# Kernel tuning notes

Measured on AMD Instinct MI355X. Metric: run time of the kernel, lower is better.

The kernel has to match this reference:

```python
import jax, jax.numpy as jnp
import numpy as np
from jax.scipy.special import ndtr

EPS1 = 1e-6
WEIGHT_DECAY = 1e-5  # FLAGS.weight_decay


def setup_inputs() -> dict:
    key = jax.random.key(0)
    ks = jax.random.split(key, 12)
    B, F, C, Z, S = 512, 512, 500, 64, 100  # batch, features, classes (r_dim), z_dim, n_sample
    lim = np.sqrt(6.0 / (C + Z))
    def glorot(k, shape):
        fan_in, fan_out = shape
        s = np.sqrt(2.0 / (fan_in + fan_out))
        return jax.random.normal(k, shape, jnp.float32) * s
    return {
        "input_X": jax.random.normal(ks[0], (B, F), jnp.float32),
        "input_Y": (jax.random.uniform(ks[1], (B, C)) < 0.1).astype(jnp.float32),  # multi-label targets
        "noise": jax.random.normal(ks[2], (S, B, Z), jnp.float32),
        "W1": glorot(ks[3], (F, 128)), "b1": jnp.zeros((128,), jnp.float32),
        "W2": glorot(ks[4], (128, 256)), "b2": jnp.zeros((256,), jnp.float32),
        "W3": glorot(ks[5], (256, 256)), "b3": jnp.zeros((256,), jnp.float32),
        "Wmu": glorot(ks[6], (256, C)), "bmu": jnp.zeros((C,), jnp.float32),
        "r_sqrt_sigma": jax.random.uniform(ks[7], (C, Z), jnp.float32, -lim, lim),
    }


def reference(input_X, input_Y, noise, W1, b1, W2, b2, W3, b3, Wmu, bmu, r_sqrt_sigma):
    # MLP trunk
    h = jax.nn.relu(input_X @ W1 + b1)
    h = jax.nn.relu(h @ W2 + b2)
    feature = jax.nn.relu(h @ W3 + b3)

    # low-rank covariance: sigma = R R^T, covariance = sigma + I
    cov_diag = jnp.sum(r_sqrt_sigma * r_sqrt_sigma, axis=1) + 1.0  # [C]

    normalized_mu = feature @ Wmu + bmu            # [B, C]
    r_mu = normalized_mu * jnp.sqrt(cov_diag)      # [B, C]

    # MC samples of latent r: [S, B, C]
    sample_r = jnp.einsum('sbz,cz->sbc', noise, r_sqrt_sigma) + r_mu

    E = ndtr(sample_r) * (1.0 - EPS1) + EPS1 * 0.5  # probit CDF, clamped
    # logprob = sum_c [ Y*log(E) + (1-Y)*log(1-E) ]  (== -sum sample_nll)
    logprob = jnp.sum(jnp.log(E) * input_Y + jnp.log1p(-E) * (1.0 - input_Y), axis=2)  # [S, B]
    maxlogprob = jnp.max(logprob, axis=0)                       # [B]
    Eprob = jnp.mean(jnp.exp(logprob - maxlogprob), axis=0)     # [B]
    nll_loss = jnp.mean(-jnp.log(Eprob) - maxlogprob)

    # marginal (independent) probit approximated by scaled sigmoid
    indiv_prob = jax.nn.sigmoid(normalized_mu * 1.70169) * (1.0 - EPS1) + 0.5 * EPS1
    cross_entropy = jnp.log(indiv_prob) * input_Y + jnp.log1p(-indiv_prob) * (1.0 - input_Y)
    marginal_loss = -jnp.mean(jnp.sum(cross_entropy, axis=1))

    l2_loss = WEIGHT_DECAY * (jnp.sum(W1 * W1) + jnp.sum(W2 * W2)
                              + jnp.sum(W3 * W3) + jnp.sum(Wmu * Wmu))
    total_loss = l2_loss + nll_loss
    return indiv_prob, nll_loss, marginal_loss, l2_loss, total_loss
```

## Files before the change

### kernel.cpp

```cpp
#include <hip/hip_runtime.h>
#include <cstddef>

#define EPS1f 1e-6f
#define WDf   1e-5f

constexpr int Bsz = 512, Csz = 500, Zsz = 64, Ssz = 100;

typedef short bf16x8 __attribute__((ext_vector_type(8)));
typedef float f32x4 __attribute__((ext_vector_type(4)));

__device__ inline short f2bf(float f) {
  union { float f; unsigned u; } v; v.f = f;
  unsigned r = (v.u + 0x7fffu + ((v.u >> 16) & 1u)) >> 16;
  return (short)r;
}

__device__ inline float log_probit(float t) {
  const float u = t * -0.70710678118654752f;
  const float au = fabsf(u);
  const float s = __builtin_amdgcn_rcpf(fmaf(0.3275911f, au, 1.f));
  float p = fmaf(1.061405429f, s, -1.453152027f);
  p = fmaf(p, s, 1.421413741f);
  p = fmaf(p, s, -0.284496736f);
  p = fmaf(p, s, 0.254829592f);
  p = p * s;
  const float e = __expf(-au * au);
  const float f = p * e;
  const float erfc_u = (u < 0.f) ? (2.f - f) : f;
  const float E = fmaf(0.5f * erfc_u, 1.f - EPS1f, 0.5f * EPS1f);
  return __logf(E);
}

__device__ inline float block_reduce_sum(float v, float* red) {
  #pragma unroll
  for (int off = 32; off > 0; off >>= 1) v += __shfl_down(v, off, 64);
  const int lane = threadIdx.x & 63, wid = threadIdx.x >> 6;
  if (lane == 0) red[wid] = v;
  __syncthreads();
  float r = 0.f;
  if (threadIdx.x == 0) {
    const int nw = blockDim.x >> 6;
    for (int i = 0; i < nw; ++i) r += red[i];
  }
  __syncthreads();
  return r;
}

__device__ __forceinline__ void gemm32_body(
    const float* __restrict__ A, const float* __restrict__ W,
    const float* __restrict__ bias, float* __restrict__ out,
    int M, int N, int K, int bn0, int bm0, float* As_, float* Ws_, bool relu) {
  const int tid = threadIdx.x;
  const int bn = bn0 * 32, bm = bm0 * 32;
  const int sm = tid >> 3, sk4 = (tid & 7) * 4;
  const int sk = tid >> 3, sn4 = (tid & 7) * 4;
  const int tn = tid & 15, tm = tid >> 4;
  #define AS_(b, k, m) As_[(b) * 1152 + (k) * 36 + (m)]
  #define WS_(b, k, n) Ws_[(b) * 1152 + (k) * 36 + (n)]
  auto loadW = [&](int kt, float4& wv) {
    const float* wrow = W + (size_t)(kt + sk) * N;
    const int nn = bn + sn4;
    if (nn + 3 < N) wv = *reinterpret_cast<const float4*>(wrow + nn);
    else {
      wv.x = (nn + 0 < N) ? wrow[nn + 0] : 0.f;
      wv.y = (nn + 1 < N) ? wrow[nn + 1] : 0.f;
      wv.z = (nn + 2 < N) ? wrow[nn + 2] : 0.f;
      wv.w = (nn + 3 < N) ? wrow[nn + 3] : 0.f;
    }
  };
  {
    float4 av = *reinterpret_cast<const float4*>(A + (size_t)(bm + sm) * K + sk4);
    float4 wv; loadW(0, wv);
    AS_(0, sk4 + 0, sm) = av.x; AS_(0, sk4 + 1, sm) = av.y;
    AS_(0, sk4 + 2, sm) = av.z; AS_(0, sk4 + 3, sm) = av.w;
    *reinterpret_cast<float4*>(&WS_(0, sk, sn4)) = wv;
  }
  __syncthreads();
  float acc[2][2] = {};
  int pb = 0;
  for (int kt = 0; kt < K; kt += 32) {
    const bool more = (kt + 32) < K;
    float4 av2, wv2;
    if (more) {
      av2 = *reinterpret_cast<const float4*>(A + (size_t)(bm + sm) * K + kt + 32 + sk4);
      loadW(kt + 32, wv2);
    }
    #pragma unroll
    for (int k = 0; k < 32; ++k) {
      const float2 a = *reinterpret_cast<const float2*>(&AS_(pb, k, tm * 2));
      const float2 w = *reinterpret_cast<const float2*>(&WS_(pb, k, tn * 2));
      acc[0][0] = fmaf(a.x, w.x, acc[0][0]);
      acc[0][1] = fmaf(a.x, w.y, acc[0][1]);
      acc[1][0] = fmaf(a.y, w.x, acc[1][0]);
      acc[1][1] = fmaf(a.y, w.y, acc[1][1]);
    }
    if (more) {
      const int nb = pb ^ 1;
      AS_(nb, sk4 + 0, sm) = av2.x; AS_(nb, sk4 + 1, sm) = av2.y;
      AS_(nb, sk4 + 2, sm) = av2.z; AS_(nb, sk4 + 3, sm) = av2.w;
      *reinterpret_cast<float4*>(&WS_(nb, sk, sn4)) = wv2;
      __syncthreads();
      pb = nb;
    }
  }
  #pragma unroll
  for (int j = 0; j < 2; ++j) {
    const int n = bn + tn * 2 + j;
    if (n >= N) continue;
    const float bv = bias[n];
    #pragma unroll
    for (int i = 0; i < 2; ++i) {
      const int m = bm + tm * 2 + i;
      float v = acc[i][j] + bv;
      if (relu) v = fmaxf(v, 0.f);
      out[(size_t)m * N + n] = v;
    }
  }
  #undef AS_
  #undef WS_
}

__global__ __launch_bounds__(256) void prep_kernel(
    const float* __restrict__ noise, short* __restrict__ nfB,
    const float* __restrict__ R, short* __restrict__ RbF, float* __restrict__ sqrtcov,
    const float* __restrict__ X, const float* __restrict__ W1,
    const float* __restrict__ b1, float* __restrict__ h1,
    const float* __restrict__ W2, const float* __restrict__ W3,
    const float* __restrict__ Wmu, float* __restrict__ l2_part,
    float* __restrict__ rmuP, float* __restrict__ snP) {
  __shared__ float smem[2304 * 2];
  const int blk = blockIdx.x;
  const int tid = threadIdx.x;
  if (blk < 800) {
    const int g = blk * 256 + tid;
    const int s = g >> 11;
    const int r = g & 2047;
    const int bt = r >> 6;
    const int ln = r & 63;
    const int cl = ln & 15, grp = ln >> 4;
    const float* src = noise + ((size_t)(s * 512 + bt * 16 + cl) * 64 + grp * 8);
    const float4 a = *reinterpret_cast<const float4*>(src);
    const float4 b = *reinterpret_cast<const float4*>(src + 4);
    const float4 c = *reinterpret_cast<const float4*>(src + 32);
    const float4 d = *reinterpret_cast<const float4*>(src + 36);
    bf16x8* dst = reinterpret_cast<bf16x8*>(nfB);
    const int u = (s * 32 + bt) * 128 + ln;
    dst[u]      = bf16x8{ f2bf(a.x), f2bf(a.y), f2bf(a.z), f2bf(a.w),
                          f2bf(b.x), f2bf(b.y), f2bf(b.z), f2bf(b.w) };
    dst[u + 64] = bf16x8{ f2bf(c.x), f2bf(c.y), f2bf(c.z), f2bf(c.w),
                          f2bf(d.x), f2bf(d.y), f2bf(d.z), f2bf(d.w) };
  } else if (blk < 808) {
    const int idx = (blk - 800) * 256 + tid;
    const int c = idx >> 2;
    const int zq = (idx & 3) * 16;
    const bool cv = c < Csz;
    const float* src = R + (size_t)c * Zsz + zq;
    float ss = 0.f;
    if (cv) {
      #pragma unroll
      for (int q = 0; q < 4; ++q) {
        const float4 r4 = *reinterpret_cast<const float4*>(src + q * 4);
        ss = fmaf(r4.x, r4.x, ss); ss = fmaf(r4.y, r4.y, ss);
        ss = fmaf(r4.z, r4.z, ss); ss = fmaf(r4.w, r4.w, ss);
      }
    }
    ss += __shfl_xor(ss, 1, 64);
    ss += __shfl_xor(ss, 2, 64);
    if ((idx & 3) == 0 && cv) sqrtcov[c] = sqrtf(1.f + ss);
  } else if (blk < 824) {
    const int e = (blk - 808) * 256 + tid;
    const int ct = e >> 7;
    const int f = (e >> 6) & 1;
    const int lane = e & 63;
    const int cl = lane & 15, grp = lane >> 4;
    const int c = ct * 16 + cl;
    bf16x8 out = {0, 0, 0, 0, 0, 0, 0, 0};
    if (c < Csz) {
      const float* src = R + (size_t)c * Zsz + f * 32 + grp * 8;
      const float4 a = *reinterpret_cast<const float4*>(src);
      const float4 b = *reinterpret_cast<const float4*>(src + 4);
      out = bf16x8{ f2bf(a.x), f2bf(a.y), f2bf(a.z), f2bf(a.w),
                    f2bf(b.x), f2bf(b.y), f2bf(b.z), f2bf(b.w) };
    }
    reinterpret_cast<bf16x8*>(RbF)[e] = out;
  } else if (blk < 888) {
    const int bid = blk - 824;
    const int gid = bid * 256 + tid;
    const int stride = 64 * 256;
    float s = 0.f;
    for (int i = gid; i < 65536; i += stride) { float v = W1[i]; s = fmaf(v, v, s); }
    for (int i = gid; i < 32768; i += stride) { float v = W2[i]; s = fmaf(v, v, s); }
    for (int i = gid; i < 65536; i += stride) { float v = W3[i]; s = fmaf(v, v, s); }
    for (int i = gid; i < 128000; i += stride) { float v = Wmu[i]; s = fmaf(v, v, s); }
    const float tot = block_reduce_sum(s, smem);
    if (tid == 0) l2_part[bid] = tot;
  } else if (blk < 952) {
    const int idx = blk - 888;
    gemm32_body(X, W1, b1, h1, 512, 128, 512, idx & 3, idx >> 2,
                smem, smem + 2304, true);
  } else {
    const int g = (blk - 952) * 256 + tid;
    const int m = g >> 4;
    const int n = 496 + (g & 15);
    const int idx = ((n >> 4) * 32 + (m >> 4)) * 256
                  + (((n >> 2) & 3) * 16 + (m & 15)) * 4 + (n & 3);
    rmuP[idx] = 0.f;
    snP[idx] = 1.f;
  }
}

template <bool RELU>
__global__ __launch_bounds__(256) void gemm32(
    const float* __restrict__ A, const float* __restrict__ W,
    const float* __restrict__ bias, float* __restrict__ out,
    int M, int N, int K) {
  __shared__ float smem[2304 * 2];
  gemm32_body(A, W, bias, out, M, N, K, blockIdx.x, blockIdx.y,
              smem, smem + 2304, RELU);
}

__global__ __launch_bounds__(256) void gemm32_mu(
    const float* __restrict__ A, const float* __restrict__ W,
    const float* __restrict__ bias, const float* __restrict__ Y,
    const float* __restrict__ sqrtcov,
    float* __restrict__ out_prob, float* __restrict__ rmuP, float* __restrict__ snP,
    float* __restrict__ ce_part, int M, int N, int K) {
  __shared__ float As[2][32][36];
  __shared__ float Ws[2][32][36];
  const int tid = threadIdx.x;
  const int bn = blockIdx.x * 32, bm = blockIdx.y * 32;
  const int sm = tid >> 3, sk4 = (tid & 7) * 4;
  const int sk = tid >> 3, sn4 = (tid & 7) * 4;
  const int tn = tid & 15, tm = tid >> 4;

  auto loadW = [&](int kt, float4& wv) {
    const float* wrow = W + (size_t)(kt + sk) * N;
    const int nn = bn + sn4;
    if (nn + 3 < N) wv = *reinterpret_cast<const float4*>(wrow + nn);
    else {
      wv.x = (nn + 0 < N) ? wrow[nn + 0] : 0.f;
      wv.y = (nn + 1 < N) ? wrow[nn + 1] : 0.f;
      wv.z = (nn + 2 < N) ? wrow[nn + 2] : 0.f;
      wv.w = (nn + 3 < N) ? wrow[nn + 3] : 0.f;
    }
  };
  {
    float4 av = *reinterpret_cast<const float4*>(A + (size_t)(bm + sm) * K + sk4);
    float4 wv; loadW(0, wv);
    As[0][sk4 + 0][sm] = av.x; As[0][sk4 + 1][sm] = av.y;
    As[0][sk4 + 2][sm] = av.z; As[0][sk4 + 3][sm] = av.w;
    *reinterpret_cast<float4*>(&Ws[0][sk][sn4]) = wv;
  }
  __syncthreads();
  float acc[2][2] = {};
  int pb = 0;
  for (int kt = 0; kt < K; kt += 32) {
    const bool more = (kt + 32) < K;
    float4 av2, wv2;
    if (more) {
      av2 = *reinterpret_cast<const float4*>(A + (size_t)(bm + sm) * K + kt + 32 + sk4);
      loadW(kt + 32, wv2);
    }
    #pragma unroll
    for (int k = 0; k < 32; ++k) {
      const float2 a = *reinterpret_cast<const float2*>(&As[pb][k][tm * 2]);
      const float2 w = *reinterpret_cast<const float2*>(&Ws[pb][k][tn * 2]);
      acc[0][0] = fmaf(a.x, w.x, acc[0][0]);
      acc[0][1] = fmaf(a.x, w.y, acc[0][1]);
      acc[1][0] = fmaf(a.y, w.x, acc[1][0]);
      acc[1][1] = fmaf(a.y, w.y, acc[1][1]);
    }
    if (more) {
      const int nb = pb ^ 1;
      As[nb][sk4 + 0][sm] = av2.x; As[nb][sk4 + 1][sm] = av2.y;
      As[nb][sk4 + 2][sm] = av2.z; As[nb][sk4 + 3][sm] = av2.w;
      *reinterpret_cast<float4*>(&Ws[nb][sk][sn4]) = wv2;
      __syncthreads();
      pb = nb;
    }
  }
  float ce2[2] = {0.f, 0.f};
  #pragma unroll
  for (int i = 0; i < 2; ++i) {
    const int m = bm + tm * 2 + i;
    #pragma unroll
    for (int j = 0; j < 2; ++j) {
      const int n = bn + tn * 2 + j;
      if (n < N) {
        const float v = acc[i][j] + bias[n];
        const float sp = __builtin_amdgcn_rcpf(1.f + __expf(-1.70169f * v));
        const float p = fmaf(sp, 1.f - EPS1f, 0.5f * EPS1f);
        const float q = fmaf(1.f - sp, 1.f - EPS1f, 0.5f * EPS1f);
        const float y = Y[(size_t)m * N + n];
        out_prob[(size_t)m * N + n] = p;
        ce2[i] += __logf((y > 0.5f) ? p : q);
        const int idx = (((n >> 4) * 32 + (m >> 4)) << 8)
                      + ((((n >> 2) & 3) * 16 + (m & 15)) << 2) + (n & 3);
        rmuP[idx] = v * sqrtcov[n];
        snP[idx] = (y > 0.5f) ? 1.f : -1.f;
      }
    }
  }
  #pragma unroll
  for (int off = 1; off < 16; off <<= 1) {
    ce2[0] += __shfl_xor(ce2[0], off, 64);
    ce2[1] += __shfl_xor(ce2[1], off, 64);
  }
  if (tn == 0) {
    const int m0 = bm + tm * 2;
    ce_part[(size_t)blockIdx.x * Bsz + m0] = ce2[0];
    ce_part[(size_t)blockIdx.x * Bsz + m0 + 1] = ce2[1];
  }
}

__global__ __launch_bounds__(256, 6) void logprob_s2(
    const short* __restrict__ nfB, const short* __restrict__ RbF,
    const float* __restrict__ rmuP, const float* __restrict__ snP,
    float* __restrict__ lp2) {
  const int blk = blockIdx.x;
  const int btg = blk & 15;
  const int s = blk >> 4;
  const int wid = threadIdx.x >> 6;
  const int lane = threadIdx.x & 63;
  const int bt = btg * 2 + (wid & 1);
  const int ch = wid >> 1;

  const bf16x8* nf = reinterpret_cast<const bf16x8*>(nfB);
  const int nbase = (s * 32 + bt) * 128 + lane;
  const bf16x8 n0 = nf[nbase];
  const bf16x8 n1 = nf[nbase + 64];
  const bf16x8* rf = reinterpret_cast<const bf16x8*>(RbF);

  float lpl = 0.f;
  #pragma unroll 2
  for (int t = 0; t < 16; ++t) {
    const int ct = ch * 16 + t;
    const bf16x8 Rf0 = rf[(ct * 2 + 0) * 64 + lane];
    const bf16x8 Rf1 = rf[(ct * 2 + 1) * 64 + lane];
    f32x4 acc = {0.f, 0.f, 0.f, 0.f};
    acc = __builtin_amdgcn_mfma_f32_16x16x32_bf16(Rf0, n0, acc, 0, 0, 0);
    acc = __builtin_amdgcn_mfma_f32_16x16x32_bf16(Rf1, n1, acc, 0, 0, 0);
    const int fb = (ct * 32 + bt) * 256 + lane * 4;
    const float4 rmu4 = *reinterpret_cast<const float4*>(rmuP + fb);
    const float4 sn4  = *reinterpret_cast<const float4*>(snP + fb);
    lpl += log_probit((acc[0] + rmu4.x) * sn4.x);
    lpl += log_probit((acc[1] + rmu4.y) * sn4.y);
    lpl += log_probit((acc[2] + rmu4.z) * sn4.z);
    lpl += log_probit((acc[3] + rmu4.w) * sn4.w);
  }
  lpl += __shfl_xor(lpl, 16, 64);
  lpl += __shfl_xor(lpl, 32, 64);
  if (lane < 16) {
    const float fix = (ch == 1) ? 8.317766166719343f : 0.f;
    lp2[(size_t)(ch * Ssz + s) * 512 + bt * 16 + lane] = lpl + fix;
  }
}

__global__ __launch_bounds__(256) void nll_kernel(const float* __restrict__ lp2,
                                                  float* __restrict__ nll_b) {
  __shared__ float sm[4][64], sse[4][64];
  const int bl = threadIdx.x & 63;
  const int sc = threadIdx.x >> 6;
  const int b = blockIdx.x * 64 + bl;
  float m = -3.0e38f, se = 0.f;
  for (int s = sc * 25; s < sc * 25 + 25; ++s) {
    const float v = lp2[(size_t)s * 512 + b] + lp2[(size_t)(Ssz + s) * 512 + b];
    const float mn = fmaxf(m, v);
    se = se * __expf(m - mn) + __expf(v - mn);
    m = mn;
  }
  sm[sc][bl] = m; sse[sc][bl] = se;
  __syncthreads();
  if (sc == 0) {
    float M = sm[0][bl];
    #pragma unroll
    for (int i = 1; i < 4; ++i) M = fmaxf(M, sm[i][bl]);
    float SE = 0.f;
    #pragma unroll
    for (int i = 0; i < 4; ++i) SE += sse[i][bl] * __expf(sm[i][bl] - M);
    nll_b[b] = -__logf(SE * (1.f / (float)Ssz)) - M;
  }
}

__global__ __launch_bounds__(256) void finals_kernel(
    const float* __restrict__ nll_b, const float* __restrict__ ce_part,
    const float* __restrict__ l2_part, int nparts, float* __restrict__ out4) {
  __shared__ float red[4];
  const int t = threadIdx.x;
  const float snll = block_reduce_sum(nll_b[t] + nll_b[t + 256], red);
  float ce = 0.f;
  #pragma unroll
  for (int i = 0; i < 32; ++i) ce += ce_part[i * 256 + t];
  const float sce = block_reduce_sum(ce, red);
  const float sl2 = block_reduce_sum((t < nparts) ? l2_part[t] : 0.f, red);
  if (t == 0) {
    const float nll = snll / (float)Bsz;
    const float marg = -sce / (float)Bsz;
    const float l2v = WDf * sl2;
    out4[0] = nll;
    out4[1] = marg;
    out4[2] = l2v;
    out4[3] = l2v + nll;
  }
}

extern "C" void kernel_launch(void* const* d_in, const int* in_sizes, int n_in,
                              void* d_out, int out_size, void* d_ws, size_t ws_size,
                              hipStream_t stream) {
  const float* X = (const float*)d_in[0];
  const float* Y = (const float*)d_in[1];
  const float* noise = (const float*)d_in[2];
  const float* W1 = (const float*)d_in[3];
  const float* b1 = (const float*)d_in[4];
  const float* W2 = (const float*)d_in[5];
  const float* b2 = (const float*)d_in[6];
  const float* W3 = (const float*)d_in[7];
  const float* b3 = (const float*)d_in[8];
  const float* Wmu = (const float*)d_in[9];
  const float* bmu = (const float*)d_in[10];
  const float* rss = (const float*)d_in[11];

  float* ws = (float*)d_ws;
  float* h1 = ws;
  float* h2 = h1 + 65536;
  float* feat = h2 + 131072;
  float* B0 = ws + 327680;
  float* sqrtcov = B0;
  float* rmuP = sqrtcov + 512;
  float* snP = rmuP + 262144;
  float* ce_part = snP + 262144;
  float* nll_b = ce_part + 8192;
  float* l2_part = nll_b + 512;
  float* lp2 = l2_part + 128;
  short* RbF = (short*)(lp2 + 102400);
  short* nfB = RbF + 32768;

  float* out_prob = (float*)d_out;
  float* out4 = out_prob + (size_t)Bsz * Csz;

  prep_kernel<<<dim3(984), 256, 0, stream>>>(noise, nfB, rss, RbF, sqrtcov,
                                             X, W1, b1, h1, W2, W3, Wmu, l2_part,
                                             rmuP, snP);

  gemm32<true><<<dim3(8, 16), 256, 0, stream>>>(h1, W2, b2, h2, 512, 256, 128);
  gemm32<true><<<dim3(8, 16), 256, 0, stream>>>(h2, W3, b3, feat, 512, 256, 256);
  gemm32_mu<<<dim3(16, 16), 256, 0, stream>>>(feat, Wmu, bmu, Y, sqrtcov,
                                              out_prob, rmuP, snP, ce_part, 512, 500, 256);

  logprob_s2<<<dim3(1600), 256, 0, stream>>>(nfB, RbF, rmuP, snP, lp2);
  nll_kernel<<<dim3(8), 256, 0, stream>>>(lp2, nll_b);

  finals_kernel<<<dim3(1), 256, 0, stream>>>(nll_b, ce_part, l2_part, 64, out4);
}
```

Baseline: 83.98 us.

## Split logprob over four class chunks and fold probit constants into log2 form

```diff
diff --git a/kernel.cpp b/kernel.cpp
--- a/kernel.cpp
+++ b/kernel.cpp
@@ -13,22 +13,6 @@
   union { float f; unsigned u; } v; v.f = f;
   unsigned r = (v.u + 0x7fffu + ((v.u >> 16) & 1u)) >> 16;
   return (short)r;
-}
-
-__device__ inline float log_probit(float t) {
-  const float u = t * -0.70710678118654752f;
-  const float au = fabsf(u);
-  const float s = __builtin_amdgcn_rcpf(fmaf(0.3275911f, au, 1.f));
-  float p = fmaf(1.061405429f, s, -1.453152027f);
-  p = fmaf(p, s, 1.421413741f);
-  p = fmaf(p, s, -0.284496736f);
-  p = fmaf(p, s, 0.254829592f);
-  p = p * s;
-  const float e = __expf(-au * au);
-  const float f = p * e;
-  const float erfc_u = (u < 0.f) ? (2.f - f) : f;
-  const float E = fmaf(0.5f * erfc_u, 1.f - EPS1f, 0.5f * EPS1f);
-  return __logf(E);
 }
 
 __device__ inline float block_reduce_sum(float v, float* red) {
@@ -205,7 +189,7 @@
     const int idx = ((n >> 4) * 32 + (m >> 4)) * 256
                   + (((n >> 2) & 3) * 16 + (m & 15)) * 4 + (n & 3);
     rmuP[idx] = 0.f;
-    snP[idx] = 1.f;
+    snP[idx] = -0.70710678f;
   }
 }
 
@@ -297,7 +281,7 @@
         const int idx = (((n >> 4) * 32 + (m >> 4)) << 8)
                       + ((((n >> 2) & 3) * 16 + (m & 15)) << 2) + (n & 3);
         rmuP[idx] = v * sqrtcov[n];
-        snP[idx] = (y > 0.5f) ? 1.f : -1.f;
+        snP[idx] = (y > 0.5f) ? -0.70710678f : 0.70710678f;
       }
     }
   }
@@ -313,17 +297,18 @@
   }
 }
 
-__global__ __launch_bounds__(256, 6) void logprob_s2(
+__global__ __launch_bounds__(256) void logprob_s3(
     const short* __restrict__ nfB, const short* __restrict__ RbF,
     const float* __restrict__ rmuP, const float* __restrict__ snP,
-    float* __restrict__ lp2) {
+    float* __restrict__ lp4) {
   const int blk = blockIdx.x;
-  const int btg = blk & 15;
-  const int s = blk >> 4;
+  const int chh = blk & 1;
+  const int btg = (blk >> 1) & 15;
+  const int s = blk >> 5;
   const int wid = threadIdx.x >> 6;
   const int lane = threadIdx.x & 63;
   const int bt = btg * 2 + (wid & 1);
-  const int ch = wid >> 1;
+  const int chq = chh * 2 + (wid >> 1);
 
   const bf16x8* nf = reinterpret_cast<const bf16x8*>(nfB);
   const int nbase = (s * 32 + bt) * 128 + lane;
@@ -333,8 +318,8 @@
 
   float lpl = 0.f;
   #pragma unroll 2
-  for (int t = 0; t < 16; ++t) {
-    const int ct = ch * 16 + t;
+  for (int t = 0; t < 8; ++t) {
+    const int ct = chq * 8 + t;
     const bf16x8 Rf0 = rf[(ct * 2 + 0) * 64 + lane];
     const bf16x8 Rf1 = rf[(ct * 2 + 1) * 64 + lane];
     f32x4 acc = {0.f, 0.f, 0.f, 0.f};
@@ -343,20 +328,41 @@
     const int fb = (ct * 32 + bt) * 256 + lane * 4;
     const float4 rmu4 = *reinterpret_cast<const float4*>(rmuP + fb);
     const float4 sn4  = *reinterpret_cast<const float4*>(snP + fb);
-    lpl += log_probit((acc[0] + rmu4.x) * sn4.x);
-    lpl += log_probit((acc[1] + rmu4.y) * sn4.y);
-    lpl += log_probit((acc[2] + rmu4.z) * sn4.z);
-    lpl += log_probit((acc[3] + rmu4.w) * sn4.w);
+    float u[4], sc[4], p[4], e[4];
+    u[0] = (acc[0] + rmu4.x) * sn4.x;
+    u[1] = (acc[1] + rmu4.y) * sn4.y;
+    u[2] = (acc[2] + rmu4.z) * sn4.z;
+    u[3] = (acc[3] + rmu4.w) * sn4.w;
+    #pragma unroll
+    for (int i = 0; i < 4; ++i)
+      sc[i] = __builtin_amdgcn_rcpf(fmaf(0.3275911f, fabsf(u[i]), 1.f));
+    #pragma unroll
+    for (int i = 0; i < 4; ++i) {
+      float q = fmaf(0.5307027145f, sc[i], -0.7265760135f);
+      q = fmaf(q, sc[i], 0.7107068705f);
+      q = fmaf(q, sc[i], -0.142248368f);
+      q = fmaf(q, sc[i], 0.127414796f);
+      p[i] = q * sc[i];
+    }
+    #pragma unroll
+    for (int i = 0; i < 4; ++i) e[i] = __expf(-u[i] * u[i]);
+    #pragma unroll
+    for (int i = 0; i < 4; ++i) {
+      const float f = p[i] * e[i];
+      const float Phi = (u[i] < 0.f) ? 1.f - f : f;
+      lpl += __log2f(fmaf(Phi, 1.f - EPS1f, 0.5f * EPS1f));
+    }
   }
   lpl += __shfl_xor(lpl, 16, 64);
   lpl += __shfl_xor(lpl, 32, 64);
   if (lane < 16) {
-    const float fix = (ch == 1) ? 8.317766166719343f : 0.f;
-    lp2[(size_t)(ch * Ssz + s) * 512 + bt * 16 + lane] = lpl + fix;
-  }
-}
-
-__global__ __launch_bounds__(256) void nll_kernel(const float* __restrict__ lp2,
+    const float fix = (chq == 3) ? 12.0f : 0.f;
+    lp4[(size_t)(chq * Ssz + s) * 512 + bt * 16 + lane] =
+        (lpl + fix) * 0.69314718055994531f;
+  }
+}
+
+__global__ __launch_bounds__(256) void nll_kernel(const float* __restrict__ lp4,
                                                   float* __restrict__ nll_b) {
   __shared__ float sm[4][64], sse[4][64];
   const int bl = threadIdx.x & 63;
@@ -364,7 +370,10 @@
   const int b = blockIdx.x * 64 + bl;
   float m = -3.0e38f, se = 0.f;
   for (int s = sc * 25; s < sc * 25 + 25; ++s) {
-    const float v = lp2[(size_t)s * 512 + b] + lp2[(size_t)(Ssz + s) * 512 + b];
+    const float v = lp4[(size_t)s * 512 + b]
+                  + lp4[(size_t)(Ssz + s) * 512 + b]
+                  + lp4[(size_t)(2 * Ssz + s) * 512 + b]
+                  + lp4[(size_t)(3 * Ssz + s) * 512 + b];
     const float mn = fmaxf(m, v);
     se = se * __expf(m - mn) + __expf(v - mn);
     m = mn;
@@ -431,8 +440,8 @@
   float* ce_part = snP + 262144;
   float* nll_b = ce_part + 8192;
   float* l2_part = nll_b + 512;
-  float* lp2 = l2_part + 128;
-  short* RbF = (short*)(lp2 + 102400);
+  float* lp4 = l2_part + 128;
+  short* RbF = (short*)(lp4 + 204800);
   short* nfB = RbF + 32768;
 
   float* out_prob = (float*)d_out;
@@ -447,8 +456,8 @@
   gemm32_mu<<<dim3(16, 16), 256, 0, stream>>>(feat, Wmu, bmu, Y, sqrtcov,
                                               out_prob, rmuP, snP, ce_part, 512, 500, 256);
 
-  logprob_s2<<<dim3(1600), 256, 0, stream>>>(nfB, RbF, rmuP, snP, lp2);
-  nll_kernel<<<dim3(8), 256, 0, stream>>>(lp2, nll_b);
+  logprob_s3<<<dim3(3200), 256, 0, stream>>>(nfB, RbF, rmuP, snP, lp4);
+  nll_kernel<<<dim3(8), 256, 0, stream>>>(lp4, nll_b);
 
   finals_kernel<<<dim3(1), 256, 0, stream>>>(nll_b, ce_part, l2_part, 64, out4);
 }
```

New measurement: 73.69 us. -12.3%, faster.
